# Kernel optimization log

Measured on AMD Instinct MI355X. Metric: run time of the kernel, lower is better.

## Reference

```python
import jax, jax.numpy as jnp
import numpy as np

VOCAB = 50257

def setup_inputs() -> dict:
    key = jax.random.key(0)
    k1, k2, k3, k4 = jax.random.split(key, 4)
    B, T, S = 4, 4096, 8192  # batch, target_len, seq_len
    tokens = jax.random.randint(k1, (B, T), 0, VOCAB, dtype=jnp.int64)
    batch_input_ids = jax.random.randint(k2, (2, B, S), 0, VOCAB, dtype=jnp.int64)
    candidate_tokens = jax.random.randint(k3, (B, T), 0, VOCAB, dtype=jnp.int64)
    candidate_scores = jax.random.normal(k4, (B, T), dtype=jnp.float32)
    unmask_count = 4096
    return {"tokens": tokens, "batch_input_ids": batch_input_ids,
            "candidate_tokens": candidate_tokens, "candidate_scores": candidate_scores,
            "unmask_count": unmask_count}

def reference(tokens, batch_input_ids, candidate_tokens, candidate_scores, unmask_count):
    flat_scores = candidate_scores.reshape(-1)            # [N]
    flat_cand = candidate_tokens.reshape(-1)              # [N]
    flat_tok = tokens.reshape(-1)                         # [N]
    N = flat_scores.shape[0]
    idx = jnp.arange(N)
    # Stable 'better-than' matrix: strictly higher score, or equal score with lower index.
    better = (flat_scores[None, :] > flat_scores[:, None]) | (
        (flat_scores[None, :] == flat_scores[:, None]) & (idx[None, :] < idx[:, None]))
    rank = jnp.sum(better, axis=1)                        # [N] int
    selected = rank < jnp.asarray(unmask_count, dtype=rank.dtype)
    updated_flat = jnp.where(selected, flat_cand, flat_tok)
    updated_tokens = updated_flat.reshape(tokens.shape).astype(jnp.int64)
    S = batch_input_ids.shape[-1]
    T = tokens.shape[-1]
    upd = batch_input_ids
    upd = upd.at[0:1, :, S - T:S].set(updated_tokens[None])
    upd = upd.at[1:2, :, 0:T].set(updated_tokens[None])
    return updated_tokens, upd.astype(jnp.int64)
```

## Files before the change

kernel.cpp:

```cpp
#include <hip/hip_runtime.h>

#define NTOK 16384
#define BQ 4
#define TQ 4096
#define SQ 8192
#define BLK 1024
#define NBLK 16

__device__ __forceinline__ unsigned score_key(float s) {
    unsigned u = __float_as_uint(s);
    if ((u << 1) == 0u) u = 0u;
    return (u & 0x80000000u) ? ~u : (u | 0x80000000u);
}

__global__ __launch_bounds__(BLK) void token_update_kernel(
    const float* __restrict__ scores,
    const int* __restrict__ cand,
    const int* __restrict__ tok,
    const int* __restrict__ bids,
    const int* __restrict__ kptr,
    int* __restrict__ out0,
    int* __restrict__ out1)
{
    __shared__ int h0[2048 * 4];
    __shared__ int h1[128];
    __shared__ int wtot[16], wsuf[16];
    __shared__ unsigned long long s_pref;
    __shared__ int s_krem, s_E;

    const int tid  = threadIdx.x;
    const int B    = blockIdx.x;
    const int lane = tid & 63;
    const int w    = tid >> 6;

    if (tid < 512) {
        int g   = B * 512 + tid;
        int o4  = g << 2;
        int c   = o4 >> 12;
        int b   = c & 3, plane = c >> 2;
        int off = o4 & 4095;
        int addr = plane ? (BQ * SQ + b * SQ + TQ + off) : (b * SQ + off);
        *(int4*)(out1 + addr) = *(const int4*)(bids + addr);
    }

    const int K = kptr[0];
    const bool none = (K <= 0), all = (K >= NTOK);
    const bool run  = !none && !all;

    for (int t = tid; t < 2048 * 4; t += BLK) h0[t] = 0;
    if (tid == 0) { s_pref = 0ull; s_krem = 1; s_E = 1; }
    __syncthreads();

    unsigned key[16];
    const float4* s4 = (const float4*)scores;
    #pragma unroll
    for (int c = 0; c < 4; ++c) {
        float4 f = s4[c * BLK + tid];
        key[c * 4 + 0] = score_key(f.x);
        key[c * 4 + 1] = score_key(f.y);
        key[c * 4 + 2] = score_key(f.z);
        key[c * 4 + 3] = score_key(f.w);
    }
    unsigned long long pref = 0ull;
    int rbits = 35;

    if (run) {
        const int slot = tid & 3;
        #pragma unroll
        for (int j = 0; j < 16; ++j)
            atomicAdd(&h0[(key[j] >> 21) * 4 + slot], 1);
        __syncthreads();

        int4 pa = *(int4*)&h0[8 * tid];
        int4 pb = *(int4*)&h0[8 * tid + 4];
        int c0 = pa.x + pa.y + pa.z + pa.w;
        int c1 = pb.x + pb.y + pb.z + pb.w;
        int pairSum = c0 + c1;
        int incl = pairSum;
        #pragma unroll
        for (int off = 1; off < 64; off <<= 1) {
            int o = __shfl_down(incl, off, 64);
            if (lane + off < 64) incl += o;
        }
        if (lane == 0) wtot[w] = incl;
        __syncthreads();
        if (tid < 16) {
            int v = wtot[tid];
            int i2 = v;
            #pragma unroll
            for (int off = 1; off < 16; off <<= 1) {
                int o = __shfl_down(i2, off, 64);
                if (tid + off < 16) i2 += o;
            }
            wsuf[tid] = i2 - v;
        }
        __syncthreads();
        int sufPairAfter = (incl - pairSum) + wsuf[w];
        int suf1 = sufPairAfter;
        int incl1 = suf1 + c1;
        int suf0 = incl1;
        int incl0 = suf0 + c0;
        if (incl1 >= K && suf1 < K) { s_pref = (unsigned long long)(2 * tid + 1); s_krem = K - suf1; s_E = c1; }
        if (incl0 >= K && suf0 < K) { s_pref = (unsigned long long)(2 * tid + 0); s_krem = K - suf0; s_E = c0; }
        __syncthreads();

        pref = s_pref;
        int krem = s_krem, E = s_E;

        for (int L = 1; L <= 5 && krem != E; ++L) {
            int sh = 35 - 7 * L;
            if (tid < 128) h1[tid] = 0;
            __syncthreads();
            #pragma unroll
            for (int j = 0; j < 16; ++j) {
                int i = (((j >> 2) * BLK + tid) << 2) | (j & 3);
                unsigned long long P = ((unsigned long long)key[j] << 14)
                                     | (unsigned)(NTOK - 1 - i);
                if ((P >> (sh + 7)) == pref)
                    atomicAdd(&h1[(int)((P >> sh) & 127)], 1);
            }
            __syncthreads();
            if (tid < 64) {
                int d0 = h1[2 * tid], d1 = h1[2 * tid + 1];
                int T = d0 + d1;
                int inc = T;
                #pragma unroll
                for (int off = 1; off < 64; off <<= 1) {
                    int o = __shfl_down(inc, off, 64);
                    if (tid + off < 64) inc += o;
                }
                int t1 = inc - T;
                int n1 = t1 + d1;
                int t0 = n1;
                int n0 = t0 + d0;
                if (n1 >= krem && t1 < krem) { s_pref = (pref << 7) | (unsigned)(2 * tid + 1); s_krem = krem - t1; s_E = d1; }
                if (n0 >= krem && t0 < krem) { s_pref = (pref << 7) | (unsigned)(2 * tid + 0); s_krem = krem - t0; s_E = d0; }
            }
            __syncthreads();
            pref = s_pref; krem = s_krem; E = s_E;
            rbits = sh;
        }
    }

    const unsigned long long Tstar =
        none ? ~0ull : (all ? 0ull : (pref << rbits));

    if (tid < 256) {
        int i4 = B * 256 + tid;
        int i  = i4 << 2;
        float4 f = s4[i4];
        int4 c4 = ((const int4*)cand)[i4];
        int4 t4 = ((const int4*)tok)[i4];
        unsigned k0 = score_key(f.x), k1 = score_key(f.y);
        unsigned k2 = score_key(f.z), k3 = score_key(f.w);
        unsigned long long P0 = ((unsigned long long)k0 << 14) | (unsigned)(NTOK - 1 - (i + 0));
        unsigned long long P1 = ((unsigned long long)k1 << 14) | (unsigned)(NTOK - 1 - (i + 1));
        unsigned long long P2 = ((unsigned long long)k2 << 14) | (unsigned)(NTOK - 1 - (i + 2));
        unsigned long long P3 = ((unsigned long long)k3 << 14) | (unsigned)(NTOK - 1 - (i + 3));
        int4 v;
        v.x = (P0 >= Tstar) ? c4.x : t4.x;
        v.y = (P1 >= Tstar) ? c4.y : t4.y;
        v.z = (P2 >= Tstar) ? c4.z : t4.z;
        v.w = (P3 >= Tstar) ? c4.w : t4.w;
        ((int4*)out0)[i4] = v;
        int b = i >> 12, tt = i & 4095;
        *(int4*)(out1 + b * SQ + (SQ - TQ) + tt) = v;
        *(int4*)(out1 + BQ * SQ + b * SQ + tt) = v;
    }
}

extern "C" void kernel_launch(void* const* d_in, const int* in_sizes, int n_in,
                              void* d_out, int out_size, void* d_ws, size_t ws_size,
                              hipStream_t stream) {
    const int*   tok    = (const int*)d_in[0];
    const int*   bids   = (const int*)d_in[1];
    const int*   cand   = (const int*)d_in[2];
    const float* scores = (const float*)d_in[3];
    const int*   kptr   = (const int*)d_in[4];

    int* out0 = (int*)d_out;
    int* out1 = out0 + NTOK;

    token_update_kernel<<<NBLK, BLK, 0, stream>>>(
        scores, cand, tok, bids, kptr, out0, out1);
}
```

Measured before the change: 66.74 us.

## Use 11-bit radix passes with unified block-wide scan for threshold selection

Restructures the radix-select for the top-K threshold so that refinement passes use 2048-bin histograms (11 bits) instead of 128-bin (7 bits), reducing the number of possible passes. All levels share one block-wide two-pair scan. The first-level histogram uses 8 replicated slots instead of 4 to spread atomic contention, and it is zeroed with vector stores. In exchange it uses more shared memory and adds extra barriers per pass, since every pass now scans across all 16 waves.

```diff
diff --git a/kernel.cpp b/kernel.cpp
--- a/kernel.cpp
+++ b/kernel.cpp
@@ -22,8 +22,8 @@
     int* __restrict__ out0,
     int* __restrict__ out1)
 {
-    __shared__ int h0[2048 * 4];
-    __shared__ int h1[128];
+    __shared__ int h0[2048 * 8];
+    __shared__ int h1[2048];
     __shared__ int wtot[16], wsuf[16];
     __shared__ unsigned long long s_pref;
     __shared__ int s_krem, s_E;
@@ -47,7 +47,9 @@
     const bool none = (K <= 0), all = (K >= NTOK);
     const bool run  = !none && !all;
 
-    for (int t = tid; t < 2048 * 4; t += BLK) h0[t] = 0;
+    #pragma unroll
+    for (int r = 0; r < 4; ++r)
+        *(int4*)&h0[(r * BLK + tid) * 4] = make_int4(0, 0, 0, 0);
     if (tid == 0) { s_pref = 0ull; s_krem = 1; s_E = 1; }
     __syncthreads();
 
@@ -61,89 +63,84 @@
         key[c * 4 + 2] = score_key(f.z);
         key[c * 4 + 3] = score_key(f.w);
     }
+
     unsigned long long pref = 0ull;
-    int rbits = 35;
+    int rb = 35;
 
     if (run) {
-        const int slot = tid & 3;
+        const int slot = tid & 7;
         #pragma unroll
         for (int j = 0; j < 16; ++j)
-            atomicAdd(&h0[(key[j] >> 21) * 4 + slot], 1);
+            atomicAdd(&h0[(key[j] >> 21) * 8 + slot], 1);
         __syncthreads();
 
-        int4 pa = *(int4*)&h0[8 * tid];
-        int4 pb = *(int4*)&h0[8 * tid + 4];
-        int c0 = pa.x + pa.y + pa.z + pa.w;
-        int c1 = pb.x + pb.y + pb.z + pb.w;
-        int pairSum = c0 + c1;
-        int incl = pairSum;
-        #pragma unroll
-        for (int off = 1; off < 64; off <<= 1) {
-            int o = __shfl_down(incl, off, 64);
-            if (lane + off < 64) incl += o;
-        }
-        if (lane == 0) wtot[w] = incl;
-        __syncthreads();
-        if (tid < 16) {
-            int v = wtot[tid];
-            int i2 = v;
+        const int SH[5]   = {35, 24, 13, 2, 0};
+        const int BITS[5] = {11, 11, 11, 11, 2};
+        int krem = K, E = 0;
+
+        for (int L = 0; L < 5; ++L) {
+            const int sh = SH[L], bits = BITS[L];
+            int c0, c1;
+            if (L == 0) {
+                int4 a0 = *(int4*)&h0[tid * 16];
+                int4 a1 = *(int4*)&h0[tid * 16 + 4];
+                int4 b0 = *(int4*)&h0[tid * 16 + 8];
+                int4 b1 = *(int4*)&h0[tid * 16 + 12];
+                c0 = a0.x + a0.y + a0.z + a0.w + a1.x + a1.y + a1.z + a1.w;
+                c1 = b0.x + b0.y + b0.z + b0.w + b1.x + b1.y + b1.z + b1.w;
+            } else {
+                c0 = h1[2 * tid]; c1 = h1[2 * tid + 1];
+            }
+            int pairSum = c0 + c1, incl = pairSum;
             #pragma unroll
-            for (int off = 1; off < 16; off <<= 1) {
-                int o = __shfl_down(i2, off, 64);
-                if (tid + off < 16) i2 += o;
+            for (int off = 1; off < 64; off <<= 1) {
+                int o = __shfl_down(incl, off, 64);
+                if (lane + off < 64) incl += o;
             }
-            wsuf[tid] = i2 - v;
-        }
-        __syncthreads();
-        int sufPairAfter = (incl - pairSum) + wsuf[w];
-        int suf1 = sufPairAfter;
-        int incl1 = suf1 + c1;
-        int suf0 = incl1;
-        int incl0 = suf0 + c0;
-        if (incl1 >= K && suf1 < K) { s_pref = (unsigned long long)(2 * tid + 1); s_krem = K - suf1; s_E = c1; }
-        if (incl0 >= K && suf0 < K) { s_pref = (unsigned long long)(2 * tid + 0); s_krem = K - suf0; s_E = c0; }
-        __syncthreads();
+            if (lane == 0) wtot[w] = incl;
+            __syncthreads();
+            if (tid < 16) {
+                int v = wtot[tid], i2 = v;
+                #pragma unroll
+                for (int off = 1; off < 16; off <<= 1) {
+                    int o = __shfl_down(i2, off, 64);
+                    if (tid + off < 16) i2 += o;
+                }
+                wsuf[tid] = i2 - v;
+            }
+            __syncthreads();
+            int sufPair = (incl - pairSum) + wsuf[w];
+            int suf1 = sufPair,  n1 = suf1 + c1;
+            int suf0 = n1,       n0 = suf0 + c0;
+            if (n1 >= krem && suf1 < krem) {
+                s_pref = (pref << bits) | (unsigned)(2 * tid + 1);
+                s_krem = krem - suf1; s_E = c1;
+            }
+            if (n0 >= krem && suf0 < krem) {
+                s_pref = (pref << bits) | (unsigned)(2 * tid);
+                s_krem = krem - suf0; s_E = c0;
+            }
+            __syncthreads();
+            pref = s_pref; krem = s_krem; E = s_E; rb = sh;
+            if (krem == E || L == 4) break;
 
-        pref = s_pref;
-        int krem = s_krem, E = s_E;
-
-        for (int L = 1; L <= 5 && krem != E; ++L) {
-            int sh = 35 - 7 * L;
-            if (tid < 128) h1[tid] = 0;
+            h1[2 * tid] = 0; h1[2 * tid + 1] = 0;
             __syncthreads();
+            const int nsh = SH[L + 1], nbits = BITS[L + 1];
             #pragma unroll
             for (int j = 0; j < 16; ++j) {
                 int i = (((j >> 2) * BLK + tid) << 2) | (j & 3);
                 unsigned long long P = ((unsigned long long)key[j] << 14)
                                      | (unsigned)(NTOK - 1 - i);
-                if ((P >> (sh + 7)) == pref)
-                    atomicAdd(&h1[(int)((P >> sh) & 127)], 1);
+                if ((P >> (nsh + nbits)) == pref)
+                    atomicAdd(&h1[(int)((P >> nsh) & ((1 << nbits) - 1))], 1);
             }
             __syncthreads();
-            if (tid < 64) {
-                int d0 = h1[2 * tid], d1 = h1[2 * tid + 1];
-                int T = d0 + d1;
-                int inc = T;
-                #pragma unroll
-                for (int off = 1; off < 64; off <<= 1) {
-                    int o = __shfl_down(inc, off, 64);
-                    if (tid + off < 64) inc += o;
-                }
-                int t1 = inc - T;
-                int n1 = t1 + d1;
-                int t0 = n1;
-                int n0 = t0 + d0;
-                if (n1 >= krem && t1 < krem) { s_pref = (pref << 7) | (unsigned)(2 * tid + 1); s_krem = krem - t1; s_E = d1; }
-                if (n0 >= krem && t0 < krem) { s_pref = (pref << 7) | (unsigned)(2 * tid + 0); s_krem = krem - t0; s_E = d0; }
-            }
-            __syncthreads();
-            pref = s_pref; krem = s_krem; E = s_E;
-            rbits = sh;
         }
     }
 
     const unsigned long long Tstar =
-        none ? ~0ull : (all ? 0ull : (pref << rbits));
+        none ? ~0ull : (all ? 0ull : (pref << rb));
 
     if (tid < 256) {
         int i4 = B * 256 + tid;
@@ -151,12 +148,10 @@
         float4 f = s4[i4];
         int4 c4 = ((const int4*)cand)[i4];
         int4 t4 = ((const int4*)tok)[i4];
-        unsigned k0 = score_key(f.x), k1 = score_key(f.y);
-        unsigned k2 = score_key(f.z), k3 = score_key(f.w);
-        unsigned long long P0 = ((unsigned long long)k0 << 14) | (unsigned)(NTOK - 1 - (i + 0));
-        unsigned long long P1 = ((unsigned long long)k1 << 14) | (unsigned)(NTOK - 1 - (i + 1));
-        unsigned long long P2 = ((unsigned long long)k2 << 14) | (unsigned)(NTOK - 1 - (i + 2));
-        unsigned long long P3 = ((unsigned long long)k3 << 14) | (unsigned)(NTOK - 1 - (i + 3));
+        unsigned long long P0 = ((unsigned long long)score_key(f.x) << 14) | (unsigned)(NTOK - 1 - (i + 0));
+        unsigned long long P1 = ((unsigned long long)score_key(f.y) << 14) | (unsigned)(NTOK - 1 - (i + 1));
+        unsigned long long P2 = ((unsigned long long)score_key(f.z) << 14) | (unsigned)(NTOK - 1 - (i + 2));
+        unsigned long long P3 = ((unsigned long long)score_key(f.w) << 14) | (unsigned)(NTOK - 1 - (i + 3));
         int4 v;
         v.x = (P0 >= Tstar) ? c4.x : t4.x;
         v.y = (P1 >= Tstar) ? c4.y : t4.y;
```

After: 65.81 us. Within noise of the previous version (-1.4%).
